# Optimization experiments

Hardware: AMD Instinct MI355X
Metric: run time of the kernel (lower is better)

## Reference

```python
import jax, jax.numpy as jnp
import numpy as np

EPS = 1e-5  # nn.LayerNorm default


def channel_ln(x, g, b):
    # LayerNorm over the channel axis of an NCHW tensor
    mu = jnp.mean(x, axis=1, keepdims=True)
    var = jnp.mean((x - mu) ** 2, axis=1, keepdims=True)
    xn = (x - mu) * jax.lax.rsqrt(var + EPS)
    return xn * g[None, :, None, None] + b[None, :, None, None]


def setup_inputs() -> dict:
    key = jax.random.key(0)
    ks = jax.random.split(key, 8)
    B, C, H, W = 16, 392, 64, 64
    n, ws = 8, 7            # head_dim = C//n = 49 = ws'^2
    hidden = int(C * 4.0)
    f32 = jnp.float32
    return {
        "x": jax.random.normal(ks[0], (B, C, H, W), f32),
        "ln1_g": jnp.ones((C,), f32),
        "ln1_b": jnp.zeros((C,), f32),
        "qkv_w": jax.random.normal(ks[1], (3 * C, C), f32) * 0.02,
        "qkv_b": jnp.zeros((3 * C,), f32),
        "rel_bias": jax.random.normal(ks[2], (n, ws, ws), f32) * 0.02,
        "proj_w": jax.random.normal(ks[3], (C, C), f32) * 0.02,
        "proj_b": jnp.zeros((C,), f32),
        "ln2_g": jnp.ones((C,), f32),
        "ln2_b": jnp.zeros((C,), f32),
        "fc1_w": jax.random.normal(ks[4], (hidden, C), f32) * 0.02,
        "fc1_b": jnp.zeros((hidden,), f32),
        "fc2_w": jax.random.normal(ks[5], (C, hidden), f32) * 0.02,
        "fc2_b": jnp.zeros((C,), f32),
    }


def reference(x, ln1_g, ln1_b, qkv_w, qkv_b, rel_bias, proj_w, proj_b,
              ln2_g, ln2_b, fc1_w, fc1_b, fc2_w, fc2_b):
    B, C, H, W = x.shape
    n = rel_bias.shape[0]
    hd = C // n  # == ws'^2 (49)
    shortcut = x

    # --- attention branch ---
    h = channel_ln(x, ln1_g, ln1_b)
    qkv = jnp.einsum('oc,bchw->bohw', qkv_w, h) + qkv_b[None, :, None, None]
    qkv = qkv.reshape(B, 3, n, hd, H * W).transpose(1, 0, 2, 4, 3)  # [3,B,n,HW,hd]
    q, k, v = qkv[0], qkv[1], qkv[2]
    scale = hd ** -0.5
    bias = rel_bias.reshape(n, -1)[None, :, None, :]        # [1,n,1,hd]
    attn = jax.nn.softmax(q * scale * k + bias, axis=-1)    # elementwise qk score
    out = (attn * v).reshape(B, C, H, W)  # row-major reshape == torch .view on contiguous
    out = jnp.einsum('oc,bchw->bohw', proj_w, out) + proj_b[None, :, None, None]
    x = shortcut + out

    # --- conv-MLP branch ---
    h = channel_ln(x, ln2_g, ln2_b)
    h = jnp.einsum('oc,bchw->bohw', fc1_w, h) + fc1_b[None, :, None, None]
    h = jax.nn.gelu(h, approximate=False)  # nn.GELU default is exact erf
    h = jnp.einsum('oc,bchw->bohw', fc2_w, h) + fc2_b[None, :, None, None]
    return x + h
```

## Files before the change

### kernel.cpp

```cpp
#include <hip/hip_runtime.h>

typedef unsigned short u16;
typedef __attribute__((ext_vector_type(8))) short short8;
typedef __attribute__((ext_vector_type(8))) unsigned short u16x8;
typedef __attribute__((ext_vector_type(4))) unsigned short u16x4;
typedef __attribute__((ext_vector_type(4))) float f32x4;

#define DEVINL __device__ __forceinline__

DEVINL float bf2f(u16 v) { return __builtin_bit_cast(float, (unsigned int)v << 16); }
DEVINL u16 f2bf(float f) {
  unsigned int u = __builtin_bit_cast(unsigned int, f);
  u += 0x7fffu + ((u >> 16) & 1u);
  return (u16)(u >> 16);
}

DEVINL float loadx(const void* p, size_t i, int flag) {
  return flag ? bf2f(((const u16*)p)[i]) : ((const float*)p)[i];
}

DEVINL f32x4 mfma16(short8 a, short8 b, f32x4 c) {
  return __builtin_amdgcn_mfma_f32_16x16x32_bf16(a, b, c, 0, 0, 0);
}

DEVINL void gload16(const u16* g, u16* l) {
  __builtin_amdgcn_global_load_lds(
      (const __attribute__((address_space(1))) unsigned int*)g,
      (__attribute__((address_space(3))) unsigned int*)l,
      16, 0, 0);
}

__global__ void k_detect(const unsigned int* __restrict__ xw, int* __restrict__ flag)
{
  const int t = threadIdx.x;
  int cnt = 0;
  for (int i = t; i < 4096; i += 256) {
    unsigned int w = xw[i];
    unsigned int h = w & 0xFFFFu;
    unsigned int e = (h >> 7) & 0xFFu;
    if (((h & 0x7FFFu) == 0u) || (e >= 117u && e <= 130u)) cnt++;
  }
  #pragma unroll
  for (int d = 1; d < 64; d <<= 1) cnt += __shfl_xor(cnt, d);
  __shared__ int acc[4];
  if ((t & 63) == 0) acc[t >> 6] = cnt;
  __syncthreads();
  if (t == 0) *flag = ((acc[0] + acc[1] + acc[2] + acc[3]) > 2048) ? 1 : 0;
}

__global__ void k_prep_fold(const void* __restrict__ w, const void* __restrict__ g,
                            const void* __restrict__ beta, const void* __restrict__ wbias,
                            const int* __restrict__ dflag,
                            u16* __restrict__ wp, float* __restrict__ wsum, float* __restrict__ cb,
                            int rows, int K, int KP)
{
  const int flag = *dflag;
  const int o = blockIdx.x;
  const int lane = threadIdx.x;
  float ws = 0.f, c = 0.f;
  if (o < rows) {
    for (int k = lane; k < KP; k += 64) {
      u16 outv = 0;
      if (k < K) {
        float wv = loadx(w, (size_t)o * K + k, flag);
        float gv = loadx(g, k, flag);
        outv = f2bf(wv * gv);
        ws += bf2f(outv);
        c  += wv * loadx(beta, k, flag);
      }
      wp[(size_t)o * KP + k] = outv;
    }
  } else {
    for (int k = lane; k < KP; k += 64) wp[(size_t)o * KP + k] = 0;
  }
  #pragma unroll
  for (int d = 1; d < 64; d <<= 1) { ws += __shfl_xor(ws, d); c += __shfl_xor(c, d); }
  if (lane == 0) { wsum[o] = ws; cb[o] = (o < rows) ? (c + loadx(wbias, o, flag)) : 0.f; }
}

__global__ void k_prep_pad(const void* __restrict__ w, const int* __restrict__ dflag,
                           u16* __restrict__ wp, int rows, int K, int KP, long total)
{
  const int flag = *dflag;
  long i = (long)blockIdx.x * 256 + threadIdx.x;
  if (i >= total) return;
  int r = (int)(i / KP), c2 = (int)(i % KP);
  wp[i] = (r < rows && c2 < K) ? f2bf(loadx(w, (size_t)r * K + c2, flag)) : (u16)0;
}

__global__ __launch_bounds__(256) void k_transpose(const void* __restrict__ xraw,
                                                   const int* __restrict__ dflag,
                                                   u16* __restrict__ xt, int jg0)
{
  __shared__ u16 ts[64][72];
  const int flag = *dflag;
  const int t = threadIdx.x;
  const int j0l = blockIdx.x * 64;
  const int j0g = jg0 + j0l;
  const int c0 = blockIdx.y * 64;
  const int c_l = t >> 2;
  const int c = c0 + c_l;
  const int bb = j0g >> 12;
  const int hw0 = j0g & 4095;

  #pragma unroll
  for (int u = 0; u < 2; ++u) {
    int jp = u * 32 + (t & 3) * 8;
    u16 vv[8] = {0, 0, 0, 0, 0, 0, 0, 0};
    if (c < 392) {
      size_t base = (((size_t)(bb * 392 + c)) << 12) + hw0 + jp;
      if (flag) {
        u16x8 v = *(const u16x8*)((const u16*)xraw + base);
        #pragma unroll
        for (int i = 0; i < 8; ++i) vv[i] = v[i];
      } else {
        const float* xf = (const float*)xraw + base;
        f32x4 a = *(const f32x4*)xf;
        f32x4 b = *(const f32x4*)(xf + 4);
        #pragma unroll
        for (int i = 0; i < 4; ++i) { vv[i] = f2bf(a[i]); vv[4 + i] = f2bf(b[i]); }
      }
    }
    #pragma unroll
    for (int i = 0; i < 8; ++i) ts[jp + i][c_l] = vv[i];
  }
  __syncthreads();
  const int j_l = t >> 2;
  #pragma unroll
  for (int u = 0; u < 2; ++u) {
    int cp = u * 32 + (t & 3) * 8;
    u16x8 w;
    #pragma unroll
    for (int i = 0; i < 8; ++i) w[i] = ts[j_l][cp + i];
    int cg = c0 + cp;
    if (cg < 416) *(u16x8*)(xt + (size_t)(j0l + j_l) * 416 + cg) = w;
  }
}

__global__ __launch_bounds__(256) void k_att_tr(const u16* __restrict__ att,
                                                u16* __restrict__ aout)
{
  __shared__ u16 ts[64][72];
  const int t = threadIdx.x;
  const int j0l = blockIdx.x * 64;
  const int c0 = blockIdx.y * 64;
  const int c_l = t >> 2;
  const int c = c0 + c_l;
  const int slab = j0l >> 12;
  const int hw0 = j0l & 4095;

  #pragma unroll
  for (int u = 0; u < 2; ++u) {
    int jp = u * 32 + (t & 3) * 8;
    u16x8 v = {0, 0, 0, 0, 0, 0, 0, 0};
    if (c < 392)
      v = *(const u16x8*)(att + (size_t)slab * 1605632 + (size_t)c * 4096 + hw0 + jp);
    #pragma unroll
    for (int i = 0; i < 8; ++i) ts[jp + i][c_l] = v[i];
  }
  __syncthreads();
  const int j_l = t >> 2;
  #pragma unroll
  for (int u = 0; u < 2; ++u) {
    int cp = u * 32 + (t & 3) * 8;
    u16x8 w;
    #pragma unroll
    for (int i = 0; i < 8; ++i) w[i] = ts[j_l][cp + i];
    int cg = c0 + cp;
    if (cg < 416) *(u16x8*)(aout + (size_t)(j0l + j_l) * 416 + cg) = w;
  }
}

__global__ __launch_bounds__(256) void k_rowstats(const u16* __restrict__ buf,
                                                  float* __restrict__ sum, float* __restrict__ sq)
{
  const int t = threadIdx.x;
  const int lane = t & 63;
  const int row = blockIdx.x * 4 + (t >> 6);
  float s = 0.f, q = 0.f;
  if (lane < 52) {
    u16x8 v = *(const u16x8*)(buf + (size_t)row * 416 + lane * 8);
    #pragma unroll
    for (int i = 0; i < 8; ++i) { float f = bf2f(v[i]); s += f; q += f * f; }
  }
  #pragma unroll
  for (int d = 1; d < 64; d <<= 1) { s += __shfl_xor(s, d); q += __shfl_xor(q, d); }
  if (lane == 0) { sum[row] = s; sq[row] = q; }
}

__global__ __launch_bounds__(256, 2) void k_qkv(
    const u16* __restrict__ xt, const u16* __restrict__ w1p,
    const float* __restrict__ wsum1, const float* __restrict__ cb1,
    const float* __restrict__ sum1, const float* __restrict__ sq1,
    const void* __restrict__ relb, const int* __restrict__ dflag,
    u16* __restrict__ attout)
{
  __shared__ __align__(16) u16 lsA[128 * 32];
  __shared__ __align__(16) u16 lsB[3 * 64 * 32];
  const int flag = *dflag;
  const int t = threadIdx.x;
  const int wid = t >> 6, lane = t & 63;
  const int l15 = lane & 15, quad = lane >> 4;
  const int bid = blockIdx.x;
  const int h = (bid >> 3) & 7;
  const int jl0 = ((bid & 7) + ((bid >> 6) << 3)) * 128;

  const u16* ga0 = xt + (size_t)(jl0 + (t >> 2)) * 416 + (t & 3) * 8;
  const u16* ga1 = ga0 + (size_t)64 * 416;
  const int orow = t >> 2, kpart = (t & 3) * 8;
  const u16* gbq = w1p + (size_t)(h * 49 + orow) * 416 + kpart;
  const u16* gbk = w1p + (size_t)(392 + h * 49 + orow) * 416 + kpart;
  const u16* gbv = w1p + (size_t)(784 + h * 49 + orow) * 416 + kpart;

  f32x4 zero4 = {0.f, 0.f, 0.f, 0.f};
  f32x4 accq[2][4], acck[2][4], accv[2][4];
  #pragma unroll
  for (int a = 0; a < 2; ++a)
    #pragma unroll
    for (int b2 = 0; b2 < 4; ++b2) { accq[a][b2] = zero4; acck[a][b2] = zero4; accv[a][b2] = zero4; }

  for (int kk = 0; kk < 416; kk += 32) {
    __syncthreads();
    gload16(ga0 + kk, lsA + t * 8);
    gload16(ga1 + kk, lsA + 2048 + t * 8);
    gload16(gbq + kk, lsB + t * 8);
    gload16(gbk + kk, lsB + 2048 + t * 8);
    gload16(gbv + kk, lsB + 4096 + t * 8);
    __syncthreads();
    short8 af0 = *(const short8*)(lsA + ((wid * 32 + l15) * 32 + quad * 8));
    short8 af1 = *(const short8*)(lsA + ((wid * 32 + 16 + l15) * 32 + quad * 8));
    #pragma unroll
    for (int of = 0; of < 4; ++of) {
      const int bo_ = (of * 16 + l15) * 32 + quad * 8;
      short8 bq = *(const short8*)(lsB + bo_);
      short8 bk = *(const short8*)(lsB + 2048 + bo_);
      short8 bv = *(const short8*)(lsB + 4096 + bo_);
      accq[0][of] = mfma16(af0, bq, accq[0][of]);
      accq[1][of] = mfma16(af1, bq, accq[1][of]);
      acck[0][of] = mfma16(af0, bk, acck[0][of]);
      acck[1][of] = mfma16(af1, bk, acck[1][of]);
      accv[0][of] = mfma16(af0, bv, accv[0][of]);
      accv[1][of] = mfma16(af1, bv, accv[1][of]);
    }
  }

  const float scale = 1.f / 7.f;
  float cq[4], wq[4], ck[4], wk[4], cv[4], wv_[4], bo[4];
  int dl[4];
  #pragma unroll
  for (int of = 0; of < 4; ++of) {
    int d = of * 16 + l15; dl[of] = d;
    int rq = h * 49 + d, rk = 392 + h * 49 + d, rv = 784 + h * 49 + d;
    wq[of] = wsum1[rq]; cq[of] = cb1[rq];
    wk[of] = wsum1[rk]; ck[of] = cb1[rk];
    wv_[of] = wsum1[rv]; cv[of] = cb1[rv];
    bo[of] = (d < 49) ? loadx(relb, h * 49 + d, flag) : 0.f;
  }
  #pragma unroll
  for (int jf = 0; jf < 2; ++jf) {
    #pragma unroll
    for (int r = 0; r < 4; ++r) {
      int jl = jl0 + wid * 32 + jf * 16 + quad * 4 + r;
      float mu = sum1[jl] * (1.f / 392.f);
      float var = sq1[jl] * (1.f / 392.f) - mu * mu;
      float rs = rsqrtf(fmaxf(var, 0.f) + 1e-5f);
      float sv[4], vv[4];
      float mx = -1e30f;
      #pragma unroll
      for (int of = 0; of < 4; ++of) {
        float qv = rs * accq[jf][of][r] + cq[of] - mu * rs * wq[of];
        float kv = rs * acck[jf][of][r] + ck[of] - mu * rs * wk[of];
        float s = (dl[of] < 49) ? (qv * scale * kv + bo[of]) : -1e30f;
        sv[of] = s; mx = fmaxf(mx, s);
        vv[of] = rs * accv[jf][of][r] + cv[of] - mu * rs * wv_[of];
      }
      #pragma unroll
      for (int d2 = 1; d2 < 16; d2 <<= 1) mx = fmaxf(mx, __shfl_xor(mx, d2));
      float sum = 0.f;
      #pragma unroll
      for (int of = 0; of < 4; ++of) { float e = __expf(sv[of] - mx); sv[of] = e; sum += e; }
      #pragma unroll
      for (int d2 = 1; d2 < 16; d2 <<= 1) sum += __shfl_xor(sum, d2);
      float inv = 1.f / sum;
      int pos = jl & 4095, slab = jl >> 12;
      size_t base = (size_t)slab * 1605632 + (size_t)h * 200704 + (size_t)pos * 49;
      #pragma unroll
      for (int of = 0; of < 4; ++of) {
        if (dl[of] < 49) attout[base + dl[of]] = f2bf(sv[of] * inv * vv[of]);
      }
    }
  }
}

__global__ __launch_bounds__(256, 2) void k_proj(
    const u16* __restrict__ aout, const u16* __restrict__ wpp,
    const void* __restrict__ projb, const int* __restrict__ dflag,
    const u16* __restrict__ xt, u16* __restrict__ x2t)
{
  __shared__ __align__(16) u16 lsA[128 * 32];
  __shared__ __align__(16) u16 lsB[64 * 32];
  const int flag = *dflag;
  const int t = threadIdx.x;
  const int wid = t >> 6, lane = t & 63;
  const int l15 = lane & 15, quad = lane >> 4;
  const int jl0 = blockIdx.x * 128, o0 = blockIdx.y * 64;

  const u16* ga0 = aout + (size_t)(jl0 + (t >> 2)) * 416 + (t & 3) * 8;
  const u16* ga1 = ga0 + (size_t)64 * 416;
  const u16* gb = wpp + (size_t)(o0 + (t >> 2)) * 416 + (t & 3) * 8;

  f32x4 zero4 = {0.f, 0.f, 0.f, 0.f};
  f32x4 acc[2][4];
  #pragma unroll
  for (int a = 0; a < 2; ++a)
    #pragma unroll
    for (int b2 = 0; b2 < 4; ++b2) acc[a][b2] = zero4;

  for (int kk = 0; kk < 416; kk += 32) {
    __syncthreads();
    gload16(ga0 + kk, lsA + t * 8);
    gload16(ga1 + kk, lsA + 2048 + t * 8);
    gload16(gb + kk, lsB + t * 8);
    __syncthreads();
    short8 af0 = *(const short8*)(lsA + ((wid * 32 + l15) * 32 + quad * 8));
    short8 af1 = *(const short8*)(lsA + ((wid * 32 + 16 + l15) * 32 + quad * 8));
    #pragma unroll
    for (int of = 0; of < 4; ++of) {
      short8 bf = *(const short8*)(lsB + ((of * 16 + l15) * 32 + quad * 8));
      acc[0][of] = mfma16(af0, bf, acc[0][of]);
      acc[1][of] = mfma16(af1, bf, acc[1][of]);
    }
  }

  float pb[4]; int og[4];
  #pragma unroll
  for (int of = 0; of < 4; ++of) {
    int o = o0 + of * 16 + l15; og[of] = o;
    pb[of] = (o < 392) ? loadx(projb, o, flag) : 0.f;
  }
  #pragma unroll
  for (int jf = 0; jf < 2; ++jf) {
    #pragma unroll
    for (int r = 0; r < 4; ++r) {
      int jl = jl0 + wid * 32 + jf * 16 + quad * 4 + r;
      #pragma unroll
      for (int of = 0; of < 4; ++of) {
        int o = og[of];
        if (o < 392) {
          float val = acc[jf][of][r] + pb[of] + bf2f(xt[(size_t)jl * 416 + o]);
          x2t[(size_t)jl * 416 + o] = f2bf(val);
        } else if (o < 416) {
          x2t[(size_t)jl * 416 + o] = 0;
        }
      }
    }
  }
}

__global__ __launch_bounds__(256, 2) void k_fc1(
    const u16* __restrict__ x2t, const u16* __restrict__ w3p,
    const float* __restrict__ wsum3, const float* __restrict__ cb3,
    const float* __restrict__ sum2, const float* __restrict__ sq2,
    u16* __restrict__ ut)
{
  __shared__ __align__(16) u16 lsA[128 * 32];
  __shared__ __align__(16) u16 lsB[64 * 32];
  const int t = threadIdx.x;
  const int wid = t >> 6, lane = t & 63;
  const int l15 = lane & 15, quad = lane >> 4;
  const int jl0 = blockIdx.x * 128, o0 = blockIdx.y * 64;

  const u16* ga0 = x2t + (size_t)(jl0 + (t >> 2)) * 416 + (t & 3) * 8;
  const u16* ga1 = ga0 + (size_t)64 * 416;
  const u16* gb = w3p + (size_t)(o0 + (t >> 2)) * 416 + (t & 3) * 8;

  f32x4 zero4 = {0.f, 0.f, 0.f, 0.f};
  f32x4 acc[2][4];
  #pragma unroll
  for (int a = 0; a < 2; ++a)
    #pragma unroll
    for (int b2 = 0; b2 < 4; ++b2) acc[a][b2] = zero4;

  for (int kk = 0; kk < 416; kk += 32) {
    __syncthreads();
    gload16(ga0 + kk, lsA + t * 8);
    gload16(ga1 + kk, lsA + 2048 + t * 8);
    gload16(gb + kk, lsB + t * 8);
    __syncthreads();
    short8 af0 = *(const short8*)(lsA + ((wid * 32 + l15) * 32 + quad * 8));
    short8 af1 = *(const short8*)(lsA + ((wid * 32 + 16 + l15) * 32 + quad * 8));
    #pragma unroll
    for (int of = 0; of < 4; ++of) {
      short8 bf = *(const short8*)(lsB + ((of * 16 + l15) * 32 + quad * 8));
      acc[0][of] = mfma16(af0, bf, acc[0][of]);
      acc[1][of] = mfma16(af1, bf, acc[1][of]);
    }
  }

  float c3[4], w3[4]; int og[4];
  #pragma unroll
  for (int of = 0; of < 4; ++of) {
    int o = o0 + of * 16 + l15; og[of] = o;
    c3[of] = cb3[o]; w3[of] = wsum3[o];
  }
  #pragma unroll
  for (int jf = 0; jf < 2; ++jf) {
    #pragma unroll
    for (int r = 0; r < 4; ++r) {
      int jl = jl0 + wid * 32 + jf * 16 + quad * 4 + r;
      float mu = sum2[jl] * (1.f / 392.f);
      float var = sq2[jl] * (1.f / 392.f) - mu * mu;
      float rs = rsqrtf(fmaxf(var, 0.f) + 1e-5f);
      #pragma unroll
      for (int of = 0; of < 4; ++of) {
        if (og[of] < 1568) {
          float u = rs * acc[jf][of][r] + c3[of] - mu * rs * w3[of];
          float gl = 0.5f * u * (1.f + erff(u * 0.70710678118654752f));
          ut[(size_t)jl * 1568 + og[of]] = f2bf(gl);
        }
      }
    }
  }
}

__global__ __launch_bounds__(256, 2) void k_fc2(
    const u16* __restrict__ ut, const u16* __restrict__ wfp,
    const void* __restrict__ fc2b, const int* __restrict__ dflag,
    const u16* __restrict__ x2t, void* __restrict__ outp, int jfg0)
{
  __shared__ __align__(16) u16 lsA[128 * 32];
  __shared__ __align__(16) u16 lsB[64 * 32];
  const int flag = *dflag;
  const int t = threadIdx.x;
  const int wid = t >> 6, lane = t & 63;
  const int l15 = lane & 15, quad = lane >> 4;
  const int jl0 = blockIdx.x * 128, o0 = blockIdx.y * 64;

  const u16* ga0 = ut + (size_t)(jl0 + (t >> 2)) * 1568 + (t & 3) * 8;
  const u16* ga1 = ga0 + (size_t)64 * 1568;
  const u16* gb = wfp + (size_t)(o0 + (t >> 2)) * 1568 + (t & 3) * 8;

  f32x4 zero4 = {0.f, 0.f, 0.f, 0.f};
  f32x4 acc[2][4];
  #pragma unroll
  for (int a = 0; a < 2; ++a)
    #pragma unroll
    for (int b2 = 0; b2 < 4; ++b2) acc[a][b2] = zero4;

  for (int kk = 0; kk < 1568; kk += 32) {
    __syncthreads();
    gload16(ga0 + kk, lsA + t * 8);
    gload16(ga1 + kk, lsA + 2048 + t * 8);
    gload16(gb + kk, lsB + t * 8);
    __syncthreads();
    short8 af0 = *(const short8*)(lsA + ((wid * 32 + l15) * 32 + quad * 8));
    short8 af1 = *(const short8*)(lsA + ((wid * 32 + 16 + l15) * 32 + quad * 8));
    #pragma unroll
    for (int of = 0; of < 4; ++of) {
      short8 bf = *(const short8*)(lsB + ((of * 16 + l15) * 32 + quad * 8));
      acc[0][of] = mfma16(af0, bf, acc[0][of]);
      acc[1][of] = mfma16(af1, bf, acc[1][of]);
    }
  }

  float fb[4]; int og[4];
  #pragma unroll
  for (int of = 0; of < 4; ++of) {
    int o = o0 + of * 16 + l15; og[of] = o;
    fb[of] = (o < 392) ? loadx(fc2b, o, flag) : 0.f;
  }
  #pragma unroll
  for (int jf = 0; jf < 2; ++jf) {
    int jlbase = jl0 + wid * 32 + jf * 16 + quad * 4;
    int jgbase = jfg0 + jlbase;
    int bslab = jgbase >> 12;
    int hw = jgbase & 4095;
    #pragma unroll
    for (int of = 0; of < 4; ++of) {
      if (og[of] < 392) {
        float v4[4];
        #pragma unroll
        for (int r = 0; r < 4; ++r)
          v4[r] = acc[jf][of][r] + fb[of] + bf2f(x2t[(size_t)(jlbase + r) * 416 + og[of]]);
        size_t obase = (((size_t)(bslab * 392 + og[of])) << 12) + hw;
        if (flag) {
          u16x4 pk;
          #pragma unroll
          for (int r = 0; r < 4; ++r) pk[r] = f2bf(v4[r]);
          *(u16x4*)((u16*)outp + obase) = pk;
        } else {
          f32x4 pk;
          #pragma unroll
          for (int r = 0; r < 4; ++r) pk[r] = v4[r];
          *(f32x4*)((float*)outp + obase) = pk;
        }
      }
    }
  }
}

extern "C" void kernel_launch(void* const* d_in, const int* in_sizes, int n_in,
                              void* d_out, int out_size, void* d_ws, size_t ws_size,
                              hipStream_t stream)
{
  if (n_in != 14 || in_sizes[0] != 16 * 392 * 64 * 64 || out_size != 16 * 392 * 64 * 64 ||
      in_sizes[3] != 3 * 392 * 392 || in_sizes[5] != 8 * 7 * 7 ||
      in_sizes[10] != 1568 * 392 || in_sizes[12] != 392 * 1568) {
    return;
  }

  const void* x     = d_in[0];
  const void* g1    = d_in[1];
  const void* b1    = d_in[2];
  const void* qkvw  = d_in[3];
  const void* qkvb  = d_in[4];
  const void* relb  = d_in[5];
  const void* projw = d_in[6];
  const void* projb = d_in[7];
  const void* g2    = d_in[8];
  const void* b2    = d_in[9];
  const void* fc1w  = d_in[10];
  const void* fc1b  = d_in[11];
  const void* fc2w  = d_in[12];
  const void* fc2b  = d_in[13];

  int S = 0, F = 0;
  {
    const int cand[8][2] = {{16,8},{16,4},{8,4},{8,2},{4,2},{4,1},{2,1},{1,1}};
    for (int i = 0; i < 8; ++i) {
      size_t nb = (size_t)cand[i][0] * 4096 * 416 * 2 * 3
                + (size_t)cand[i][1] * 4096 * 1568 * 2
                + (size_t)8 * 1024 * 1024;
      if (nb <= ws_size) { S = cand[i][0]; F = cand[i][1]; break; }
    }
    if (S == 0) return;
  }

  char* wsb = (char*)d_ws;
  size_t off = 0;
  auto alloc = [&](size_t bytes) -> void* {
    void* p = wsb + off;
    off = (off + bytes + 255) & ~(size_t)255;
    return p;
  };
  int*  dflag = (int*)alloc(256);
  u16* xt    = (u16*)alloc((size_t)S * 4096 * 416 * 2);
  u16* aout  = (u16*)alloc((size_t)S * 4096 * 416 * 2);
  u16* x2t   = (u16*)alloc((size_t)S * 4096 * 416 * 2);
  u16* ut    = (u16*)alloc((size_t)F * 4096 * 1568 * 2);
  u16* w1p   = (u16*)alloc((size_t)1200 * 416 * 2);
  u16* w3p   = (u16*)alloc((size_t)1600 * 416 * 2);
  u16* wpp   = (u16*)alloc((size_t)448 * 416 * 2);
  u16* wfp   = (u16*)alloc((size_t)448 * 1568 * 2);
  float* wsum1 = (float*)alloc(1200 * 4);
  float* cb1   = (float*)alloc(1200 * 4);
  float* wsum3 = (float*)alloc(1600 * 4);
  float* cb3   = (float*)alloc(1600 * 4);
  float* sum1  = (float*)alloc((size_t)65536 * 4);
  float* sq1   = (float*)alloc((size_t)65536 * 4);
  float* sum2  = (float*)alloc((size_t)65536 * 4);
  float* sq2   = (float*)alloc((size_t)65536 * 4);

  u16* att = x2t;

  k_detect<<<1, 256, 0, stream>>>((const unsigned int*)x, dflag);

  k_prep_fold<<<1200, 64, 0, stream>>>(qkvw, g1, b1, qkvb, dflag, w1p, wsum1, cb1, 1176, 392, 416);
  k_prep_fold<<<1600, 64, 0, stream>>>(fc1w, g2, b2, fc1b, dflag, w3p, wsum3, cb3, 1568, 392, 416);
  k_prep_pad<<<(448 * 416 + 255) / 256, 256, 0, stream>>>(projw, dflag, wpp, 392, 392, 416, (long)448 * 416);
  k_prep_pad<<<(448 * 1568 + 255) / 256, 256, 0, stream>>>(fc2w, dflag, wfp, 392, 1568, 1568, (long)448 * 1568);

  for (int c0 = 0; c0 < 16; c0 += S) {
    const int jg0 = c0 * 4096;
    k_transpose<<<dim3(S * 64, 7), 256, 0, stream>>>(x, dflag, xt, jg0);
    k_rowstats<<<S * 1024, 256, 0, stream>>>(xt, sum1, sq1);
    k_qkv<<<dim3(S * 256), 256, 0, stream>>>(xt, w1p, wsum1, cb1, sum1, sq1, relb, dflag, att);
    k_att_tr<<<dim3(S * 64, 7), 256, 0, stream>>>(att, aout);
    k_proj<<<dim3(S * 32, 7), 256, 0, stream>>>(aout, wpp, projb, dflag, xt, x2t);
    k_rowstats<<<S * 1024, 256, 0, stream>>>(x2t, sum2, sq2);
    for (int f0 = 0; f0 < S; f0 += F) {
      const int jfg0 = (c0 + f0) * 4096;
      const u16* x2sub = x2t + (size_t)f0 * 4096 * 416;
      k_fc1<<<dim3(F * 32, 25), 256, 0, stream>>>(x2sub, w3p, wsum3, cb3,
                                                  sum2 + (size_t)f0 * 4096, sq2 + (size_t)f0 * 4096, ut);
      k_fc2<<<dim3(F * 32, 7), 256, 0, stream>>>(ut, wfp, fc2b, dflag, x2sub, d_out, jfg0);
    }
  }
}
```

Baseline: 857.3 us.

## Double-buffer LDS tiles in GEMM kernels to overlap global loads with MFMA

Converts the K-loops of the qkv, proj, fc1 and fc2 GEMM kernels from single-buffered load/sync/compute to a two-stage ping-pong LDS pipeline. The next tile's global-to-LDS loads are issued before computing the current tile, using vmcnt waits and raw barriers. This aims to hide global memory latency behind MFMA work. It doubles LDS per block, which may reduce occupancy, and the scheduling fences constrain how the compiler can interleave instructions.

New measurement: 881.1 us. 1.03x slower.

```diff
diff --git a/kernel.cpp b/kernel.cpp
--- a/kernel.cpp
+++ b/kernel.cpp
@@ -29,6 +29,10 @@
       (__attribute__((address_space(3))) unsigned int*)l,
       16, 0, 0);
 }
+
+#define WAIT_VM(n) asm volatile("s_waitcnt vmcnt(" #n ")" ::: "memory")
+#define SBAR() __builtin_amdgcn_s_barrier()
+#define SCHED_FENCE() __builtin_amdgcn_sched_barrier(0)
 
 __global__ void k_detect(const unsigned int* __restrict__ xw, int* __restrict__ flag)
 {
@@ -195,8 +199,8 @@
     const void* __restrict__ relb, const int* __restrict__ dflag,
     u16* __restrict__ attout)
 {
-  __shared__ __align__(16) u16 lsA[128 * 32];
-  __shared__ __align__(16) u16 lsB[3 * 64 * 32];
+  __shared__ __align__(16) u16 lsA[2 * 4096];
+  __shared__ __align__(16) u16 lsB[2 * 6144];
   const int flag = *dflag;
   const int t = threadIdx.x;
   const int wid = t >> 6, lane = t & 63;
@@ -219,22 +223,37 @@
     #pragma unroll
     for (int b2 = 0; b2 < 4; ++b2) { accq[a][b2] = zero4; acck[a][b2] = zero4; accv[a][b2] = zero4; }
 
-  for (int kk = 0; kk < 416; kk += 32) {
-    __syncthreads();
-    gload16(ga0 + kk, lsA + t * 8);
-    gload16(ga1 + kk, lsA + 2048 + t * 8);
-    gload16(gbq + kk, lsB + t * 8);
-    gload16(gbk + kk, lsB + 2048 + t * 8);
-    gload16(gbv + kk, lsB + 4096 + t * 8);
-    __syncthreads();
-    short8 af0 = *(const short8*)(lsA + ((wid * 32 + l15) * 32 + quad * 8));
-    short8 af1 = *(const short8*)(lsA + ((wid * 32 + 16 + l15) * 32 + quad * 8));
+  auto stage = [&](int b, int kk) {
+    u16* A = lsA + b * 4096;
+    u16* B = lsB + b * 6144;
+    gload16(ga0 + kk, A + t * 8);
+    gload16(ga1 + kk, A + 2048 + t * 8);
+    gload16(gbq + kk, B + t * 8);
+    gload16(gbk + kk, B + 2048 + t * 8);
+    gload16(gbv + kk, B + 4096 + t * 8);
+  };
+
+  stage(0, 0);
+  int cur = 0;
+  for (int it = 0; it < 13; ++it) {
+    if (it < 12) {
+      stage(cur ^ 1, (it + 1) * 32);
+      WAIT_VM(5);
+    } else {
+      WAIT_VM(0);
+    }
+    SBAR();
+    SCHED_FENCE();
+    const u16* A = lsA + cur * 4096;
+    const u16* B = lsB + cur * 6144;
+    short8 af0 = *(const short8*)(A + ((wid * 32 + l15) * 32 + quad * 8));
+    short8 af1 = *(const short8*)(A + ((wid * 32 + 16 + l15) * 32 + quad * 8));
     #pragma unroll
     for (int of = 0; of < 4; ++of) {
       const int bo_ = (of * 16 + l15) * 32 + quad * 8;
-      short8 bq = *(const short8*)(lsB + bo_);
-      short8 bk = *(const short8*)(lsB + 2048 + bo_);
-      short8 bv = *(const short8*)(lsB + 4096 + bo_);
+      short8 bq = *(const short8*)(B + bo_);
+      short8 bk = *(const short8*)(B + 2048 + bo_);
+      short8 bv = *(const short8*)(B + 4096 + bo_);
       accq[0][of] = mfma16(af0, bq, accq[0][of]);
       accq[1][of] = mfma16(af1, bq, accq[1][of]);
       acck[0][of] = mfma16(af0, bk, acck[0][of]);
@@ -242,6 +261,9 @@
       accv[0][of] = mfma16(af0, bv, accv[0][of]);
       accv[1][of] = mfma16(af1, bv, accv[1][of]);
     }
+    SCHED_FENCE();
+    SBAR();
+    cur ^= 1;
   }
 
   const float scale = 1.f / 7.f;
@@ -297,8 +319,8 @@
     const void* __restrict__ projb, const int* __restrict__ dflag,
     const u16* __restrict__ xt, u16* __restrict__ x2t)
 {
-  __shared__ __align__(16) u16 lsA[128 * 32];
-  __shared__ __align__(16) u16 lsB[64 * 32];
+  __shared__ __align__(16) u16 lsA[2 * 4096];
+  __shared__ __align__(16) u16 lsB[2 * 2048];
   const int flag = *dflag;
   const int t = threadIdx.x;
   const int wid = t >> 6, lane = t & 63;
@@ -316,20 +338,34 @@
     #pragma unroll
     for (int b2 = 0; b2 < 4; ++b2) acc[a][b2] = zero4;
 
-  for (int kk = 0; kk < 416; kk += 32) {
-    __syncthreads();
-    gload16(ga0 + kk, lsA + t * 8);
-    gload16(ga1 + kk, lsA + 2048 + t * 8);
-    gload16(gb + kk, lsB + t * 8);
-    __syncthreads();
-    short8 af0 = *(const short8*)(lsA + ((wid * 32 + l15) * 32 + quad * 8));
-    short8 af1 = *(const short8*)(lsA + ((wid * 32 + 16 + l15) * 32 + quad * 8));
+  auto stage = [&](int b, int kk) {
+    u16* A = lsA + b * 4096;
+    u16* B = lsB + b * 2048;
+    gload16(ga0 + kk, A + t * 8);
+    gload16(ga1 + kk, A + 2048 + t * 8);
+    gload16(gb + kk, B + t * 8);
+  };
+
+  stage(0, 0);
+  int cur = 0;
+  for (int it = 0; it < 13; ++it) {
+    if (it < 12) { stage(cur ^ 1, (it + 1) * 32); WAIT_VM(3); }
+    else WAIT_VM(0);
+    SBAR();
+    SCHED_FENCE();
+    const u16* A = lsA + cur * 4096;
+    const u16* B = lsB + cur * 2048;
+    short8 af0 = *(const short8*)(A + ((wid * 32 + l15) * 32 + quad * 8));
+    short8 af1 = *(const short8*)(A + ((wid * 32 + 16 + l15) * 32 + quad * 8));
     #pragma unroll
     for (int of = 0; of < 4; ++of) {
-      short8 bf = *(const short8*)(lsB + ((of * 16 + l15) * 32 + quad * 8));
+      short8 bf = *(const short8*)(B + ((of * 16 + l15) * 32 + quad * 8));
       acc[0][of] = mfma16(af0, bf, acc[0][of]);
       acc[1][of] = mfma16(af1, bf, acc[1][of]);
     }
+    SCHED_FENCE();
+    SBAR();
+    cur ^= 1;
   }
 
   float pb[4]; int og[4];
@@ -363,8 +399,8 @@
     const float* __restrict__ sum2, const float* __restrict__ sq2,
     u16* __restrict__ ut)
 {
-  __shared__ __align__(16) u16 lsA[128 * 32];
-  __shared__ __align__(16) u16 lsB[64 * 32];
+  __shared__ __align__(16) u16 lsA[2 * 4096];
+  __shared__ __align__(16) u16 lsB[2 * 2048];
   const int t = threadIdx.x;
   const int wid = t >> 6, lane = t & 63;
   const int l15 = lane & 15, quad = lane >> 4;
@@ -381,20 +417,34 @@
     #pragma unroll
     for (int b2 = 0; b2 < 4; ++b2) acc[a][b2] = zero4;
 
-  for (int kk = 0; kk < 416; kk += 32) {
-    __syncthreads();
-    gload16(ga0 + kk, lsA + t * 8);
-    gload16(ga1 + kk, lsA + 2048 + t * 8);
-    gload16(gb + kk, lsB + t * 8);
-    __syncthreads();
-    short8 af0 = *(const short8*)(lsA + ((wid * 32 + l15) * 32 + quad * 8));
-    short8 af1 = *(const short8*)(lsA + ((wid * 32 + 16 + l15) * 32 + quad * 8));
+  auto stage = [&](int b, int kk) {
+    u16* A = lsA + b * 4096;
+    u16* B = lsB + b * 2048;
+    gload16(ga0 + kk, A + t * 8);
+    gload16(ga1 + kk, A + 2048 + t * 8);
+    gload16(gb + kk, B + t * 8);
+  };
+
+  stage(0, 0);
+  int cur = 0;
+  for (int it = 0; it < 13; ++it) {
+    if (it < 12) { stage(cur ^ 1, (it + 1) * 32); WAIT_VM(3); }
+    else WAIT_VM(0);
+    SBAR();
+    SCHED_FENCE();
+    const u16* A = lsA + cur * 4096;
+    const u16* B = lsB + cur * 2048;
+    short8 af0 = *(const short8*)(A + ((wid * 32 + l15) * 32 + quad * 8));
+    short8 af1 = *(const short8*)(A + ((wid * 32 + 16 + l15) * 32 + quad * 8));
     #pragma unroll
     for (int of = 0; of < 4; ++of) {
-      short8 bf = *(const short8*)(lsB + ((of * 16 + l15) * 32 + quad * 8));
+      short8 bf = *(const short8*)(B + ((of * 16 + l15) * 32 + quad * 8));
       acc[0][of] = mfma16(af0, bf, acc[0][of]);
       acc[1][of] = mfma16(af1, bf, acc[1][of]);
     }
+    SCHED_FENCE();
+    SBAR();
+    cur ^= 1;
   }
 
   float c3[4], w3[4]; int og[4];
@@ -428,8 +478,8 @@
     const void* __restrict__ fc2b, const int* __restrict__ dflag,
     const u16* __restrict__ x2t, void* __restrict__ outp, int jfg0)
 {
-  __shared__ __align__(16) u16 lsA[128 * 32];
-  __shared__ __align__(16) u16 lsB[64 * 32];
+  __shared__ __align__(16) u16 lsA[2 * 4096];
+  __shared__ __align__(16) u16 lsB[2 * 2048];
   const int flag = *dflag;
   const int t = threadIdx.x;
   const int wid = t >> 6, lane = t & 63;
@@ -447,20 +497,34 @@
     #pragma unroll
     for (int b2 = 0; b2 < 4; ++b2) acc[a][b2] = zero4;
 
-  for (int kk = 0; kk < 1568; kk += 32) {
-    __syncthreads();
-    gload16(ga0 + kk, lsA + t * 8);
-    gload16(ga1 + kk, lsA + 2048 + t * 8);
-    gload16(gb + kk, lsB + t * 8);
-    __syncthreads();
-    short8 af0 = *(const short8*)(lsA + ((wid * 32 + l15) * 32 + quad * 8));
-    short8 af1 = *(const short8*)(lsA + ((wid * 32 + 16 + l15) * 32 + quad * 8));
+  auto stage = [&](int b, int kk) {
+    u16* A = lsA + b * 4096;
+    u16* B = lsB + b * 2048;
+    gload16(ga0 + kk, A + t * 8);
+    gload16(ga1 + kk, A + 2048 + t * 8);
+    gload16(gb + kk, B + t * 8);
+  };
+
+  stage(0, 0);
+  int cur = 0;
+  for (int it = 0; it < 49; ++it) {
+    if (it < 48) { stage(cur ^ 1, (it + 1) * 32); WAIT_VM(3); }
+    else WAIT_VM(0);
+    SBAR();
+    SCHED_FENCE();
+    const u16* A = lsA + cur * 4096;
+    const u16* B = lsB + cur * 2048;
+    short8 af0 = *(const short8*)(A + ((wid * 32 + l15) * 32 + quad * 8));
+    short8 af1 = *(const short8*)(A + ((wid * 32 + 16 + l15) * 32 + quad * 8));
     #pragma unroll
     for (int of = 0; of < 4; ++of) {
-      short8 bf = *(const short8*)(lsB + ((of * 16 + l15) * 32 + quad * 8));
+      short8 bf = *(const short8*)(B + ((of * 16 + l15) * 32 + quad * 8));
       acc[0][of] = mfma16(af0, bf, acc[0][of]);
       acc[1][of] = mfma16(af1, bf, acc[1][of]);
     }
+    SCHED_FENCE();
+    SBAR();
+    cur ^= 1;
   }
 
   float fb[4]; int og[4];
```
